# Optimization experiments

Measured on AMD Instinct MI355X. Metric: run time of the kernel, lower is better.

Reference implementation:

```python
import math
import jax, jax.numpy as jnp
import numpy as np

NB, NF, NTS = 16, 512, 2048
FREQ_START, FREQ_END = 0.1, 10.0
C = 1.0 / (8.0 * math.pi ** 2)


def setup_inputs() -> dict:
    key = jax.random.key(0)
    k1, k2 = jax.random.split(key)
    ys = jax.random.normal(k1, (NB, NTS), dtype=jnp.float32)
    # irregular but monotonically increasing time stamps in [0, NTS)
    ts = jnp.sort(jax.random.uniform(k2, (NB, NTS), dtype=jnp.float32,
                                     minval=0.0, maxval=float(NTS)), axis=1)
    freq = jnp.linspace(FREQ_START, FREQ_END, NF, dtype=jnp.float32)
    return {"ys": ys, "ts": ts, "freq": freq}


def reference(ys, ts, freq):
    nts = ts.shape[1]
    # center of the window: midpoint of the two central samples -> [B,1,1]
    tau = (0.5 * (ts[:, nts // 2] + ts[:, nts // 2 + 1]))[:, None, None]
    omega = freq * (2.0 * math.pi)            # [F]
    omega_ = omega[None, :, None]             # [1,F,1]
    ts_ = ts[:, None, :]                      # [B,1,T]
    ys_ = ys[:, None, :]                      # [B,1,T]

    dz = omega_ * (ts_ - tau)                 # [B,F,T]
    weights = jnp.exp(-C * dz * dz)           # shared Gaussian window [B,F,T]
    sum_w = jnp.sum(weights, axis=-1)         # [B,F]

    def w_mean(x):
        return jnp.sum(weights * x, axis=-1) / sum_w

    theta = omega_ * ts_
    sin_basis = jnp.sin(theta)
    cos_basis = jnp.cos(theta)

    sin_one = w_mean(sin_basis)
    cos_one = w_mean(cos_basis)
    sin_cos = w_mean(sin_basis * cos_basis)
    sin_sin = w_mean(sin_basis * sin_basis)
    cos_cos = w_mean(cos_basis * cos_basis)

    numerator = 2.0 * (sin_cos - sin_one * cos_one)
    denominator = cos_cos - cos_one ** 2 - (sin_sin - sin_one ** 2)
    time_shift = jnp.arctan2(numerator, denominator) / (2.0 * omega)  # [B,F]

    phase_arg = omega_ * (ts_ - time_shift[:, :, None])
    sin_shift = jnp.sin(phase_arg)
    cos_shift = jnp.cos(phase_arg)
    sin_tau_center = jnp.sin(omega * (time_shift - tau[:, :, 0]))  # [B,F]
    cos_tau_center = jnp.cos(omega * (time_shift - tau[:, :, 0]))

    ys_cos_shift = w_mean(ys_ * cos_shift)
    ys_sin_shift = w_mean(ys_ * sin_shift)
    ys_one = w_mean(ys_)
    cos_shift_one = w_mean(cos_shift)
    sin_shift_one = w_mean(sin_shift)

    A = 2.0 * (ys_cos_shift - ys_one * cos_shift_one)
    B = 2.0 * (ys_sin_shift - ys_one * sin_shift_one)

    a0 = ys_one
    a1 = cos_tau_center * A - sin_tau_center * B
    a2 = sin_tau_center * A + cos_tau_center * B
    wwp = a1 ** 2 + a2 ** 2
    phase = jnp.arctan2(a2, a1)
    return (wwp, phase, a0, a1, a2)
```

## Files before the change

### kernel.cpp

```cpp
#include <hip/hip_runtime.h>
#include <math.h>

namespace {
constexpr int kNB  = 16;
constexpr int kNF  = 512;
constexpr int kNTS = 2048;
constexpr int kTPB = 256;
constexpr int kEPT = kNTS / kTPB;
constexpr int kVPT = kEPT / 4;
constexpr float kC     = 0.012665147955292222f;
constexpr float kTwoPi = 6.28318530717958647692f;
}

__device__ __forceinline__ void fast_sincosf(float x, float& s_out, float& c_out) {
  constexpr float kTwoOverPi = 0.636619772367581343f;
  constexpr float kP1 = 1.5703125f;
  constexpr float kP2 = 4.84466552734375e-4f;
  constexpr float kP3 = -6.407499313354492e-7f;
  constexpr float kP4 = 9.895302355289459e-10f;

  float kf = rintf(x * kTwoOverPi);
  int   q  = (int)kf;
  float r  = fmaf(-kf, kP1, x);
  r = fmaf(-kf, kP2, r);
  r = fmaf(-kf, kP3, r);
  r = fmaf(-kf, kP4, r);

  float z = r * r;
  float sp = fmaf(fmaf(-1.9515295891e-4f, z, 8.3321608736e-3f), z, -1.6666654611e-1f);
  float s  = fmaf(sp * z, r, r);
  float cp = fmaf(fmaf(2.443315711809948e-5f, z, -1.388731625493765e-3f), z,
                  4.166664568298827e-2f);
  float c  = fmaf(cp, z * z, fmaf(-0.5f, z, 1.0f));

  bool sw = (q & 1) != 0;
  float ss = sw ? c : s;
  float cc = sw ? s : c;
  unsigned sgn_s = (unsigned)(q & 2) << 30;
  unsigned sgn_c = (unsigned)((q + 1) & 2) << 30;
  s_out = __uint_as_float(__float_as_uint(ss) ^ sgn_s);
  c_out = __uint_as_float(__float_as_uint(cc) ^ sgn_c);
}

__launch_bounds__(kTPB)
__global__ void wavelet_ls_kernel(const float* __restrict__ ys,
                                  const float* __restrict__ ts,
                                  const float* __restrict__ freq,
                                  float* __restrict__ out) {
  const int f    = blockIdx.x;
  const int b    = blockIdx.y;
  const int tid  = threadIdx.x;
  const int wave = tid >> 6;

  const float* __restrict__ tsb = ts + b * kNTS;
  const float* __restrict__ ysb = ys + b * kNTS;
  const float4* __restrict__ ts4 = (const float4*)tsb;
  const float4* __restrict__ ys4 = (const float4*)ysb;

  const float tau   = 0.5f * (tsb[kNTS / 2] + tsb[kNTS / 2 + 1]);
  const float omega = freq[f] * kTwoPi;

  float tv[kEPT], yv[kEPT], wv[kEPT];

#pragma unroll
  for (int v = 0; v < kVPT; ++v) {
    const int vidx = v * kTPB + tid;
    const float4 t4 = ts4[vidx];
    const float4 y4 = ys4[vidx];
    tv[v * 4 + 0] = t4.x; tv[v * 4 + 1] = t4.y; tv[v * 4 + 2] = t4.z; tv[v * 4 + 3] = t4.w;
    yv[v * 4 + 0] = y4.x; yv[v * 4 + 1] = y4.y; yv[v * 4 + 2] = y4.z; yv[v * 4 + 3] = y4.w;
  }

  float acc[6];
#pragma unroll
  for (int i = 0; i < 6; ++i) acc[i] = 0.0f;

#pragma unroll
  for (int k = 0; k < kEPT; ++k) {
    const float t = tv[k];
    const float y = yv[k];
    const float dz = omega * (t - tau);
    const float e  = (-kC * dz) * dz;
    const float w  = __expf(e);
    wv[k] = w;
    float sn, cs;
    fast_sincosf(omega * t, sn, cs);
    const float c2 = fmaf(-2.0f * sn, sn, 1.0f);
    acc[0] += w;
    acc[1] = fmaf(w, sn, acc[1]);
    acc[2] = fmaf(w, cs, acc[2]);
    acc[3] = fmaf(w, sn * cs, acc[3]);
    acc[4] = fmaf(w, c2, acc[4]);
    acc[5] = fmaf(w, y, acc[5]);
  }

  __shared__ float lds1[4][6];
#pragma unroll
  for (int i = 0; i < 6; ++i) {
    float v = acc[i];
#pragma unroll
    for (int off = 1; off < 64; off <<= 1) v += __shfl_xor(v, off, 64);
    if ((tid & 63) == 0) lds1[wave][i] = v;
  }
  __syncthreads();

  float tot[6];
#pragma unroll
  for (int i = 0; i < 6; ++i)
    tot[i] = (lds1[0][i] + lds1[1][i]) + (lds1[2][i] + lds1[3][i]);

  const float sum_w   = tot[0];
  const float inv_w   = 1.0f / sum_w;
  const float sin_one = tot[1] * inv_w;
  const float cos_one = tot[2] * inv_w;
  const float sin_cos = tot[3] * inv_w;
  const float cc_ss   = tot[4] * inv_w;
  const float ys_one  = tot[5] * inv_w;

  const float num = 2.0f * (sin_cos - sin_one * cos_one);
  const float den = cc_ss - cos_one * cos_one + sin_one * sin_one;
  const float time_shift = atan2f(num, den) / (2.0f * omega);

  float acc2[4];
#pragma unroll
  for (int i = 0; i < 4; ++i) acc2[i] = 0.0f;

#pragma unroll
  for (int k = 0; k < kEPT; ++k) {
    float sn, cs;
    fast_sincosf(omega * (tv[k] - time_shift), sn, cs);
    const float w = wv[k];
    acc2[0] = fmaf(w, cs, acc2[0]);
    acc2[1] = fmaf(w, sn, acc2[1]);
    acc2[2] = fmaf(w, yv[k] * cs, acc2[2]);
    acc2[3] = fmaf(w, yv[k] * sn, acc2[3]);
  }

  __shared__ float lds2[4][4];
#pragma unroll
  for (int i = 0; i < 4; ++i) {
    float v = acc2[i];
#pragma unroll
    for (int off = 1; off < 64; off <<= 1) v += __shfl_xor(v, off, 64);
    if ((tid & 63) == 0) lds2[wave][i] = v;
  }
  __syncthreads();

  if (tid == 0) {
    float t2[4];
#pragma unroll
    for (int i = 0; i < 4; ++i)
      t2[i] = (lds2[0][i] + lds2[1][i]) + (lds2[2][i] + lds2[3][i]);

    const float cos_shift_one = t2[0] * inv_w;
    const float sin_shift_one = t2[1] * inv_w;
    const float ys_cos_shift  = t2[2] * inv_w;
    const float ys_sin_shift  = t2[3] * inv_w;

    float stc, ctc;
    sincosf(omega * (time_shift - tau), &stc, &ctc);

    const float A  = 2.0f * (ys_cos_shift - ys_one * cos_shift_one);
    const float B  = 2.0f * (ys_sin_shift - ys_one * sin_shift_one);
    const float a0 = ys_one;
    const float a1 = ctc * A - stc * B;
    const float a2 = stc * A + ctc * B;
    const float wwp   = a1 * a1 + a2 * a2;
    const float phase = atan2f(a2, a1);

    const int o = b * kNF + f;
    out[0 * kNB * kNF + o] = wwp;
    out[1 * kNB * kNF + o] = phase;
    out[2 * kNB * kNF + o] = a0;
    out[3 * kNB * kNF + o] = a1;
    out[4 * kNB * kNF + o] = a2;
  }
}

extern "C" void kernel_launch(void* const* d_in, const int* in_sizes, int n_in,
                              void* d_out, int out_size, void* d_ws, size_t ws_size,
                              hipStream_t stream) {
  const float* ys   = (const float*)d_in[0];
  const float* ts   = (const float*)d_in[1];
  const float* freq = (const float*)d_in[2];
  float* out = (float*)d_out;

  dim3 grid(kNF, kNB);
  wavelet_ls_kernel<<<grid, kTPB, 0, stream>>>(ys, ts, freq, out);
}
```

Measured before the change: 39.83 us.

## Assign one wavefront per frequency bin and recompute weights instead of caching

Each wavefront now handles a full (batch, frequency) bin, with four bins per block. This removes the LDS exchange and both block-level __syncthreads, leaving only wavefront shuffle reductions. Inputs are streamed in chunks and reloaded in the second pass rather than held in registers, and the Gaussian weight exp is recomputed there. The aim is lower register pressure and no cross-wave synchronisation, at the cost of four times more work per thread, extra global/cache loads and duplicated exp computation.

```diff
diff --git a/kernel.cpp b/kernel.cpp
--- a/kernel.cpp
+++ b/kernel.cpp
@@ -6,19 +6,19 @@
 constexpr int kNF  = 512;
 constexpr int kNTS = 2048;
 constexpr int kTPB = 256;
-constexpr int kEPT = kNTS / kTPB;
-constexpr int kVPT = kEPT / 4;
+constexpr int kBinsPerBlock = 4;
+constexpr int kChunks = kNTS / 4 / 64;
 constexpr float kC     = 0.012665147955292222f;
 constexpr float kTwoPi = 6.28318530717958647692f;
+
+constexpr float kTwoOverPi = 0.636619772367581343f;
+constexpr float kP1 = 1.5703125f;
+constexpr float kP2 = 4.84466552734375e-4f;
+constexpr float kP3 = -6.407499313354492e-7f;
+constexpr float kP4 = 9.895302355289459e-10f;
 }
 
 __device__ __forceinline__ void fast_sincosf(float x, float& s_out, float& c_out) {
-  constexpr float kTwoOverPi = 0.636619772367581343f;
-  constexpr float kP1 = 1.5703125f;
-  constexpr float kP2 = 4.84466552734375e-4f;
-  constexpr float kP3 = -6.407499313354492e-7f;
-  constexpr float kP4 = 9.895302355289459e-10f;
-
   float kf = rintf(x * kTwoOverPi);
   int   q  = (int)kf;
   float r  = fmaf(-kf, kP1, x);
@@ -47,10 +47,12 @@
                                   const float* __restrict__ ts,
                                   const float* __restrict__ freq,
                                   float* __restrict__ out) {
-  const int f    = blockIdx.x;
-  const int b    = blockIdx.y;
   const int tid  = threadIdx.x;
   const int wave = tid >> 6;
+  const int lane = tid & 63;
+  const int bin  = blockIdx.x * kBinsPerBlock + wave;
+  const int b    = bin >> 9;
+  const int f    = bin & (kNF - 1);
 
   const float* __restrict__ tsb = ts + b * kNTS;
   const float* __restrict__ ysb = ys + b * kNTS;
@@ -60,102 +62,98 @@
   const float tau   = 0.5f * (tsb[kNTS / 2] + tsb[kNTS / 2 + 1]);
   const float omega = freq[f] * kTwoPi;
 
-  float tv[kEPT], yv[kEPT], wv[kEPT];
-
-#pragma unroll
-  for (int v = 0; v < kVPT; ++v) {
-    const int vidx = v * kTPB + tid;
-    const float4 t4 = ts4[vidx];
-    const float4 y4 = ys4[vidx];
-    tv[v * 4 + 0] = t4.x; tv[v * 4 + 1] = t4.y; tv[v * 4 + 2] = t4.z; tv[v * 4 + 3] = t4.w;
-    yv[v * 4 + 0] = y4.x; yv[v * 4 + 1] = y4.y; yv[v * 4 + 2] = y4.z; yv[v * 4 + 3] = y4.w;
-  }
-
   float acc[6];
 #pragma unroll
   for (int i = 0; i < 6; ++i) acc[i] = 0.0f;
 
 #pragma unroll
-  for (int k = 0; k < kEPT; ++k) {
-    const float t = tv[k];
-    const float y = yv[k];
-    const float dz = omega * (t - tau);
-    const float e  = (-kC * dz) * dz;
-    const float w  = __expf(e);
-    wv[k] = w;
-    float sn, cs;
-    fast_sincosf(omega * t, sn, cs);
-    const float c2 = fmaf(-2.0f * sn, sn, 1.0f);
-    acc[0] += w;
-    acc[1] = fmaf(w, sn, acc[1]);
-    acc[2] = fmaf(w, cs, acc[2]);
-    acc[3] = fmaf(w, sn * cs, acc[3]);
-    acc[4] = fmaf(w, c2, acc[4]);
-    acc[5] = fmaf(w, y, acc[5]);
+  for (int i = 0; i < kChunks; ++i) {
+    const int c = i * 64 + lane;
+    const float4 t4 = ts4[c];
+    const float4 y4 = ys4[c];
+    const float te[4] = {t4.x, t4.y, t4.z, t4.w};
+    const float ye[4] = {y4.x, y4.y, y4.z, y4.w};
+#pragma unroll
+    for (int j = 0; j < 4; ++j) {
+      const float t = te[j];
+      const float y = ye[j];
+      const float dz = omega * (t - tau);
+      const float e  = (-kC * dz) * dz;
+      const float w  = __expf(e);
+      float sn, cs;
+      fast_sincosf(omega * t, sn, cs);
+      const float c2 = fmaf(-2.0f * sn, sn, 1.0f);
+      acc[0] += w;
+      acc[1] = fmaf(w, sn, acc[1]);
+      acc[2] = fmaf(w, cs, acc[2]);
+      acc[3] = fmaf(w, sn * cs, acc[3]);
+      acc[4] = fmaf(w, c2, acc[4]);
+      acc[5] = fmaf(w, y, acc[5]);
+    }
   }
 
-  __shared__ float lds1[4][6];
 #pragma unroll
   for (int i = 0; i < 6; ++i) {
     float v = acc[i];
 #pragma unroll
     for (int off = 1; off < 64; off <<= 1) v += __shfl_xor(v, off, 64);
-    if ((tid & 63) == 0) lds1[wave][i] = v;
+    acc[i] = v;
   }
-  __syncthreads();
 
-  float tot[6];
-#pragma unroll
-  for (int i = 0; i < 6; ++i)
-    tot[i] = (lds1[0][i] + lds1[1][i]) + (lds1[2][i] + lds1[3][i]);
-
-  const float sum_w   = tot[0];
+  const float sum_w   = acc[0];
   const float inv_w   = 1.0f / sum_w;
-  const float sin_one = tot[1] * inv_w;
-  const float cos_one = tot[2] * inv_w;
-  const float sin_cos = tot[3] * inv_w;
-  const float cc_ss   = tot[4] * inv_w;
-  const float ys_one  = tot[5] * inv_w;
+  const float sin_one = acc[1] * inv_w;
+  const float cos_one = acc[2] * inv_w;
+  const float sin_cos = acc[3] * inv_w;
+  const float cc_ss   = acc[4] * inv_w;
+  const float ys_one  = acc[5] * inv_w;
 
   const float num = 2.0f * (sin_cos - sin_one * cos_one);
   const float den = cc_ss - cos_one * cos_one + sin_one * sin_one;
   const float time_shift = atan2f(num, den) / (2.0f * omega);
 
-  float acc2[4];
+  float a20 = 0.0f, a21 = 0.0f, a22 = 0.0f, a23 = 0.0f;
 #pragma unroll
-  for (int i = 0; i < 4; ++i) acc2[i] = 0.0f;
-
+  for (int i = 0; i < kChunks; ++i) {
+    const int c = i * 64 + lane;
+    const float4 t4 = ts4[c];
+    const float4 y4 = ys4[c];
+    const float te[4] = {t4.x, t4.y, t4.z, t4.w};
+    const float ye[4] = {y4.x, y4.y, y4.z, y4.w};
 #pragma unroll
-  for (int k = 0; k < kEPT; ++k) {
-    float sn, cs;
-    fast_sincosf(omega * (tv[k] - time_shift), sn, cs);
-    const float w = wv[k];
-    acc2[0] = fmaf(w, cs, acc2[0]);
-    acc2[1] = fmaf(w, sn, acc2[1]);
-    acc2[2] = fmaf(w, yv[k] * cs, acc2[2]);
-    acc2[3] = fmaf(w, yv[k] * sn, acc2[3]);
+    for (int j = 0; j < 4; ++j) {
+      const float t = te[j];
+      const float y = ye[j];
+      const float dz = omega * (t - tau);
+      const float e  = (-kC * dz) * dz;
+      const float w  = __expf(e);
+      float sn, cs;
+      fast_sincosf(omega * (t - time_shift), sn, cs);
+      const float wy = w * y;
+      a20 = fmaf(w,  cs, a20);
+      a21 = fmaf(w,  sn, a21);
+      a22 = fmaf(wy, cs, a22);
+      a23 = fmaf(wy, sn, a23);
+    }
   }
 
-  __shared__ float lds2[4][4];
+  {
+    float av[4] = {a20, a21, a22, a23};
 #pragma unroll
-  for (int i = 0; i < 4; ++i) {
-    float v = acc2[i];
+    for (int i = 0; i < 4; ++i) {
+      float v = av[i];
 #pragma unroll
-    for (int off = 1; off < 64; off <<= 1) v += __shfl_xor(v, off, 64);
-    if ((tid & 63) == 0) lds2[wave][i] = v;
+      for (int off = 1; off < 64; off <<= 1) v += __shfl_xor(v, off, 64);
+      av[i] = v;
+    }
+    a20 = av[0]; a21 = av[1]; a22 = av[2]; a23 = av[3];
   }
-  __syncthreads();
 
-  if (tid == 0) {
-    float t2[4];
-#pragma unroll
-    for (int i = 0; i < 4; ++i)
-      t2[i] = (lds2[0][i] + lds2[1][i]) + (lds2[2][i] + lds2[3][i]);
-
-    const float cos_shift_one = t2[0] * inv_w;
-    const float sin_shift_one = t2[1] * inv_w;
-    const float ys_cos_shift  = t2[2] * inv_w;
-    const float ys_sin_shift  = t2[3] * inv_w;
+  if (lane == 0) {
+    const float cos_shift_one = a20 * inv_w;
+    const float sin_shift_one = a21 * inv_w;
+    const float ys_cos_shift  = a22 * inv_w;
+    const float ys_sin_shift  = a23 * inv_w;
 
     float stc, ctc;
     sincosf(omega * (time_shift - tau), &stc, &ctc);
@@ -185,6 +183,7 @@
   const float* freq = (const float*)d_in[2];
   float* out = (float*)d_out;
 
-  dim3 grid(kNF, kNB);
+  const int nbins = kNB * kNF;
+  dim3 grid(nbins / kBinsPerBlock);
   wavelet_ls_kernel<<<grid, kTPB, 0, stream>>>(ys, ts, freq, out);
 }
```

Result: slower. 41.86 us (+5.1%).
